# Optimization experiments

Measured on AMD Instinct MI355X. Metric: run time of the kernel, lower is better.

## Reference

```python
import jax, jax.numpy as jnp
import numpy as np

N = 8192  # number of nodes


def _deg_norm(idx, n):
    # degree^{-1/2}, zero-degree clamped to 1 (DGL allow_zero_in_degree behavior)
    deg = jax.ops.segment_sum(jnp.ones(idx.shape[0], jnp.float32), idx, num_segments=n)
    return jax.lax.rsqrt(jnp.maximum(deg, 1.0))


def _graph_conv(h, src, dst, norm_src, norm_dst, W, b):
    # norm='both': scale at src, sparse sum-aggregate, scale at dst, then linear
    h = h * norm_src[:, None]
    m = jax.ops.segment_sum(h[src], dst, num_segments=h.shape[0])  # gather + scatter-add
    m = m * norm_dst[:, None]
    return m @ W + b


def setup_inputs() -> dict:
    key = jax.random.key(0)
    k = jax.random.split(key, 6)
    E = 262144
    x = jax.random.normal(k[0], (N, 256), jnp.float32)
    src = jax.random.randint(k[1], (E,), 0, N, jnp.int32)
    dst = jax.random.randint(k[2], (E,), 0, N, jnp.int32)
    W1 = jax.random.normal(k[3], (256, 128), jnp.float32) * (1.0 / np.sqrt(256))
    b1 = jnp.zeros((128,), jnp.float32)
    W2 = jax.random.normal(k[4], (128, 128), jnp.float32) * (1.0 / np.sqrt(128))
    b2 = jnp.zeros((128,), jnp.float32)
    return {"x": x, "src": src, "dst": dst, "W1": W1, "b1": b1, "W2": W2, "b2": b2}


def reference(x, src, dst, W1, b1, W2, b2):
    n = x.shape[0]
    norm_src = _deg_norm(src, n)  # out-degree norm
    norm_dst = _deg_norm(dst, n)  # in-degree norm
    # encode: GraphConv -> relu -> GraphConv  (dropout=0 -> identity)
    h = jax.nn.relu(_graph_conv(x, src, dst, norm_src, norm_dst, W1, b1))
    h = _graph_conv(h, src, dst, norm_src, norm_dst, W2, b2)
    # decode: sigmoid(h h^T), dense [N, N] reconstruction
    return jax.nn.sigmoid(h @ h.T)
```

## Files before the change

### kernel.cpp

```cpp
#include <hip/hip_runtime.h>
#include <hip/hip_bf16.h>

typedef __attribute__((ext_vector_type(8))) short short8;
typedef __attribute__((ext_vector_type(4))) float f32x4;

#define NNODES 8192
#define FDIM 128

__global__ void k_deg_int(const int* __restrict__ src, const int* __restrict__ dst,
                          int* __restrict__ cnt_s, int* __restrict__ cnt_d, int E) {
    int e = blockIdx.x * blockDim.x + threadIdx.x;
    if (e < E) {
        atomicAdd(&cnt_s[src[e]], 1);
        atomicAdd(&cnt_d[dst[e]], 1);
    }
}

__global__ void k_norms(const int* __restrict__ cnt_s, const int* __restrict__ cnt_d,
                        float* __restrict__ norm_s, float* __restrict__ norm_d, int n) {
    int i = blockIdx.x * blockDim.x + threadIdx.x;
    if (i < n) {
        norm_s[i] = rsqrtf(fmaxf((float)cnt_s[i], 1.0f));
        norm_d[i] = rsqrtf(fmaxf((float)cnt_d[i], 1.0f));
    }
}

__global__ __launch_bounds__(256) void k_scan(const int* __restrict__ cnt,
                                              int* __restrict__ row_start,
                                              int* __restrict__ cursor, int n) {
    __shared__ int partial[256];
    __shared__ int offs[257];
    int t = threadIdx.x;
    int base = t * 32;
    int local[32];
    int s = 0;
#pragma unroll
    for (int i = 0; i < 32; ++i) { local[i] = s; s += cnt[base + i]; }
    partial[t] = s;
    __syncthreads();
    if (t == 0) {
        int acc = 0;
        for (int i = 0; i < 256; ++i) { offs[i] = acc; acc += partial[i]; }
        offs[256] = acc;
    }
    __syncthreads();
    int o = offs[t];
#pragma unroll
    for (int i = 0; i < 32; ++i) {
        int v = o + local[i];
        row_start[base + i] = v;
        cursor[base + i] = v;
    }
    if (t == 0) row_start[n] = offs[256];
}

__global__ void k_fill(const int* __restrict__ src, const int* __restrict__ dst,
                       int* __restrict__ cursor, int* __restrict__ csr_src, int E) {
    int e = blockIdx.x * blockDim.x + threadIdx.x;
    if (e < E) {
        int pos = atomicAdd(&cursor[dst[e]], 1);
        csr_src[pos] = src[e];
    }
}

template<int K, int R>
__global__ void k_linear_norm(const float* __restrict__ X, const float* __restrict__ W,
                              const float* __restrict__ norm, float* __restrict__ Y) {
    int col = threadIdx.x;
    int row0 = blockIdx.x * R;
    float acc[R];
#pragma unroll
    for (int r = 0; r < R; ++r) acc[r] = 0.f;
    for (int k = 0; k < K; ++k) {
        float w = W[k * FDIM + col];
#pragma unroll
        for (int r = 0; r < R; ++r)
            acc[r] = fmaf(X[(size_t)(row0 + r) * K + k], w, acc[r]);
    }
#pragma unroll
    for (int r = 0; r < R; ++r)
        Y[(size_t)(row0 + r) * FDIM + col] = acc[r] * norm[row0 + r];
}

static __device__ inline unsigned short f2bf(float f) {
    union { float f; unsigned int u; } a; a.f = f;
    unsigned int u = a.u;
    unsigned int r = u + 0x7FFFu + ((u >> 16) & 1u);
    return (unsigned short)(r >> 16);
}

template<int MODE>
__global__ __launch_bounds__(256) void k_gather_agg(const float* __restrict__ Y,
                                                    const int* __restrict__ row_start,
                                                    const int* __restrict__ csr_src,
                                                    const float* __restrict__ nd,
                                                    const float* __restrict__ bias,
                                                    void* __restrict__ outp) {
    int t = threadIdx.x;
    int node = blockIdx.x * 8 + (t >> 5);
    int c4 = (t & 31) << 2;
    int beg = row_start[node], end = row_start[node + 1];
    f32x4 acc = {0.f, 0.f, 0.f, 0.f};
    int e = beg;
    for (; e + 1 < end; e += 2) {
        int s0 = csr_src[e], s1 = csr_src[e + 1];
        f32x4 v0 = *(const f32x4*)(Y + ((size_t)s0 << 7) + c4);
        f32x4 v1 = *(const f32x4*)(Y + ((size_t)s1 << 7) + c4);
        acc += v0;
        acc += v1;
    }
    if (e < end) {
        int s0 = csr_src[e];
        acc += *(const f32x4*)(Y + ((size_t)s0 << 7) + c4);
    }
    float scale = nd[node];
    f32x4 b = *(const f32x4*)(bias + c4);
    f32x4 v = acc * scale + b;
    if (MODE == 0) {
#pragma unroll
        for (int i = 0; i < 4; ++i) v[i] = fmaxf(v[i], 0.f);
        *(f32x4*)((float*)outp + ((size_t)node << 7) + c4) = v;
    } else {
        ushort4 u;
        u.x = f2bf(v[0]); u.y = f2bf(v[1]); u.z = f2bf(v[2]); u.w = f2bf(v[3]);
        *(ushort4*)((unsigned short*)outp + ((size_t)node << 7) + c4) = u;
    }
}

__global__ __launch_bounds__(256) void k_decode(const __hip_bfloat16* __restrict__ H,
                                                float* __restrict__ C) {
    __shared__ __align__(16) unsigned char smem[65536];
    unsigned char* sA = smem;
    unsigned char* sB = smem + 32768;
    const int ti = blockIdx.x, tj = blockIdx.y;
    const int t = threadIdx.x;
    const unsigned char* gH = (const unsigned char*)H;

#pragma unroll
    for (int i = 0; i < 8; ++i) {
        int chunk = t + i * 256;
        int row = chunk >> 4;
        int cc = (chunk & 15) << 4;
        int lofs = row * 256 + (cc ^ ((row & 7) << 4));
        *(float4*)(sA + lofs) = *(const float4*)(gH + ((size_t)(ti * 128 + row) << 8) + cc);
        *(float4*)(sB + lofs) = *(const float4*)(gH + ((size_t)(tj * 128 + row) << 8) + cc);
    }
    __syncthreads();

    const int w = t >> 6, lane = t & 63;
    const int wr = (w >> 1) * 64, wc = (w & 1) * 64;
    const int lr = lane & 15;
    const int lk = (lane >> 4) * 16;

    f32x4 acc[4][4] = {};

#pragma unroll
    for (int ks = 0; ks < 4; ++ks) {
        short8 af[4], bfr[4];
#pragma unroll
        for (int mi = 0; mi < 4; ++mi) {
            int row = wr + mi * 16 + lr;
            int off = row * 256 + ((ks * 64 + lk) ^ ((row & 7) << 4));
            af[mi] = *(const short8*)(sA + off);
        }
#pragma unroll
        for (int ni = 0; ni < 4; ++ni) {
            int row = wc + ni * 16 + lr;
            int off = row * 256 + ((ks * 64 + lk) ^ ((row & 7) << 4));
            bfr[ni] = *(const short8*)(sB + off);
        }
#pragma unroll
        for (int mi = 0; mi < 4; ++mi)
#pragma unroll
            for (int ni = 0; ni < 4; ++ni)
                acc[mi][ni] = __builtin_amdgcn_mfma_f32_16x16x32_bf16(af[mi], bfr[ni],
                                                                      acc[mi][ni], 0, 0, 0);
    }

    const int rbase = (lane >> 4) * 4;
    const int cbase = lane & 15;
#pragma unroll
    for (int mi = 0; mi < 4; ++mi) {
#pragma unroll
        for (int ni = 0; ni < 4; ++ni) {
#pragma unroll
            for (int r = 0; r < 4; ++r) {
                int row = ti * 128 + wr + mi * 16 + rbase + r;
                int col = tj * 128 + wc + ni * 16 + cbase;
                float v = acc[mi][ni][r];
                C[(size_t)row * NNODES + col] = 1.0f / (1.0f + __expf(-v));
            }
        }
    }
}

extern "C" void kernel_launch(void* const* d_in, const int* in_sizes, int n_in,
                              void* d_out, int out_size, void* d_ws, size_t ws_size,
                              hipStream_t stream) {
    const float* x  = (const float*)d_in[0];
    const int* src  = (const int*)d_in[1];
    const int* dst  = (const int*)d_in[2];
    const float* W1 = (const float*)d_in[3];
    const float* b1 = (const float*)d_in[4];
    const float* W2 = (const float*)d_in[5];
    const float* b2 = (const float*)d_in[6];
    float* out = (float*)d_out;
    const int E = in_sizes[1];

    char* ws = (char*)d_ws;
    float* norm_s    = (float*)(ws + 0);
    float* norm_d    = (float*)(ws + (32 << 10));
    int*   cnt_s     = (int*)(ws + (64 << 10));
    int*   cnt_d     = (int*)(ws + (96 << 10));
    int*   row_start = (int*)(ws + (128 << 10));
    int*   cursor    = (int*)(ws + (164 << 10));
    int*   csr_src   = (int*)(ws + (196 << 10));
    char*  big       = ws + (196 << 10) + ((size_t)E * 4);
    float* bufA      = (float*)big;
    float* bufB      = (float*)(big + (4 << 20));
    __hip_bfloat16* h2bf = (__hip_bfloat16*)(big + (8 << 20));

    hipMemsetAsync(cnt_s, 0, 64 << 10, stream);

    k_deg_int<<<(E + 255) / 256, 256, 0, stream>>>(src, dst, cnt_s, cnt_d, E);
    k_norms<<<(NNODES + 255) / 256, 256, 0, stream>>>(cnt_s, cnt_d, norm_s, norm_d, NNODES);
    k_scan<<<1, 256, 0, stream>>>(cnt_d, row_start, cursor, NNODES);
    k_fill<<<(E + 255) / 256, 256, 0, stream>>>(src, dst, cursor, csr_src, E);

    k_linear_norm<256, 16><<<NNODES / 16, 128, 0, stream>>>(x, W1, norm_s, bufA);
    k_gather_agg<0><<<NNODES / 8, 256, 0, stream>>>(bufA, row_start, csr_src, norm_d, b1, bufB);

    k_linear_norm<128, 16><<<NNODES / 16, 128, 0, stream>>>(bufB, W2, norm_s, bufA);
    k_gather_agg<1><<<NNODES / 8, 256, 0, stream>>>(bufA, row_start, csr_src, norm_d, b2, h2bf);

    k_decode<<<dim3(64, 64), 256, 0, stream>>>(h2bf, out);
}
```

Baseline: 209.9 us.

## Stage linear inputs in LDS, merge norm into scan, replace memset with kernel

Result: faster. 189.9 us (-9.5%).

```diff
diff --git a/kernel.cpp b/kernel.cpp
--- a/kernel.cpp
+++ b/kernel.cpp
@@ -6,6 +6,11 @@
 
 #define NNODES 8192
 #define FDIM 128
+
+__global__ void k_zero(int* __restrict__ p, int n) {
+    int i = blockIdx.x * blockDim.x + threadIdx.x;
+    if (i < n) p[i] = 0;
+}
 
 __global__ void k_deg_int(const int* __restrict__ src, const int* __restrict__ dst,
                           int* __restrict__ cnt_s, int* __restrict__ cnt_d, int E) {
@@ -16,26 +21,25 @@
     }
 }
 
-__global__ void k_norms(const int* __restrict__ cnt_s, const int* __restrict__ cnt_d,
-                        float* __restrict__ norm_s, float* __restrict__ norm_d, int n) {
-    int i = blockIdx.x * blockDim.x + threadIdx.x;
-    if (i < n) {
-        norm_s[i] = rsqrtf(fmaxf((float)cnt_s[i], 1.0f));
-        norm_d[i] = rsqrtf(fmaxf((float)cnt_d[i], 1.0f));
-    }
-}
-
-__global__ __launch_bounds__(256) void k_scan(const int* __restrict__ cnt,
-                                              int* __restrict__ row_start,
-                                              int* __restrict__ cursor, int n) {
+__global__ __launch_bounds__(256) void k_scan_norms(const int* __restrict__ cnt_s,
+                                                    const int* __restrict__ cnt_d,
+                                                    float* __restrict__ norm_s,
+                                                    float* __restrict__ norm_d,
+                                                    int* __restrict__ row_start,
+                                                    int* __restrict__ cursor, int n) {
     __shared__ int partial[256];
     __shared__ int offs[257];
     int t = threadIdx.x;
     int base = t * 32;
+#pragma unroll
+    for (int i = 0; i < 32; ++i) {
+        norm_s[base + i] = rsqrtf(fmaxf((float)cnt_s[base + i], 1.0f));
+        norm_d[base + i] = rsqrtf(fmaxf((float)cnt_d[base + i], 1.0f));
+    }
     int local[32];
     int s = 0;
 #pragma unroll
-    for (int i = 0; i < 32; ++i) { local[i] = s; s += cnt[base + i]; }
+    for (int i = 0; i < 32; ++i) { local[i] = s; s += cnt_d[base + i]; }
     partial[t] = s;
     __syncthreads();
     if (t == 0) {
@@ -63,23 +67,41 @@
     }
 }
 
-template<int K, int R>
-__global__ void k_linear_norm(const float* __restrict__ X, const float* __restrict__ W,
-                              const float* __restrict__ norm, float* __restrict__ Y) {
-    int col = threadIdx.x;
-    int row0 = blockIdx.x * R;
-    float acc[R];
-#pragma unroll
-    for (int r = 0; r < R; ++r) acc[r] = 0.f;
-    for (int k = 0; k < K; ++k) {
-        float w = W[k * FDIM + col];
-#pragma unroll
-        for (int r = 0; r < R; ++r)
-            acc[r] = fmaf(X[(size_t)(row0 + r) * K + k], w, acc[r]);
-    }
-#pragma unroll
-    for (int r = 0; r < R; ++r)
-        Y[(size_t)(row0 + r) * FDIM + col] = acc[r] * norm[row0 + r];
+template<int K>
+__global__ __launch_bounds__(256) void k_linear(const float* __restrict__ X,
+                                                const float* __restrict__ W,
+                                                const float* __restrict__ norm,
+                                                float* __restrict__ Y) {
+    __shared__ float xs[16][K];
+    int t = threadIdx.x;
+    int row0 = blockIdx.x * 16;
+    constexpr int K4 = K / 4;
+    constexpr int NCH = 16 * K4 / 256;
+#pragma unroll
+    for (int i = 0; i < NCH; ++i) {
+        int c = t + i * 256;
+        int r = c / K4, k4 = c % K4;
+        *(float4*)&xs[r][k4 * 4] = *(const float4*)(X + (size_t)(row0 + r) * K + k4 * 4);
+    }
+    __syncthreads();
+
+    int lane = t & 31, g = t >> 5;
+    int r0 = g * 2, r1 = g * 2 + 1;
+    int c = lane * 4;
+    f32x4 acc0 = {0.f, 0.f, 0.f, 0.f}, acc1 = {0.f, 0.f, 0.f, 0.f};
+    for (int k = 0; k < K; k += 4) {
+        f32x4 x0 = *(f32x4*)&xs[r0][k];
+        f32x4 x1 = *(f32x4*)&xs[r1][k];
+#pragma unroll
+        for (int kk = 0; kk < 4; ++kk) {
+            f32x4 w = *(const f32x4*)(W + (size_t)(k + kk) * FDIM + c);
+            acc0 += w * x0[kk];
+            acc1 += w * x1[kk];
+        }
+    }
+    float n0 = norm[row0 + r0], n1 = norm[row0 + r1];
+    *(f32x4*)(Y + (size_t)(row0 + r0) * FDIM + c) = acc0 * n0;
+    *(f32x4*)(Y + (size_t)(row0 + r1) * FDIM + c) = acc1 * n1;
 }
 
 static __device__ inline unsigned short f2bf(float f) {
@@ -220,17 +242,16 @@
     float* bufB      = (float*)(big + (4 << 20));
     __hip_bfloat16* h2bf = (__hip_bfloat16*)(big + (8 << 20));
 
-    hipMemsetAsync(cnt_s, 0, 64 << 10, stream);
+    k_zero<<<(2 * NNODES + 255) / 256, 256, 0, stream>>>(cnt_s, 2 * NNODES);
 
     k_deg_int<<<(E + 255) / 256, 256, 0, stream>>>(src, dst, cnt_s, cnt_d, E);
-    k_norms<<<(NNODES + 255) / 256, 256, 0, stream>>>(cnt_s, cnt_d, norm_s, norm_d, NNODES);
-    k_scan<<<1, 256, 0, stream>>>(cnt_d, row_start, cursor, NNODES);
+    k_scan_norms<<<1, 256, 0, stream>>>(cnt_s, cnt_d, norm_s, norm_d, row_start, cursor, NNODES);
     k_fill<<<(E + 255) / 256, 256, 0, stream>>>(src, dst, cursor, csr_src, E);
 
-    k_linear_norm<256, 16><<<NNODES / 16, 128, 0, stream>>>(x, W1, norm_s, bufA);
+    k_linear<256><<<NNODES / 16, 256, 0, stream>>>(x, W1, norm_s, bufA);
     k_gather_agg<0><<<NNODES / 8, 256, 0, stream>>>(bufA, row_start, csr_src, norm_d, b1, bufB);
 
-    k_linear_norm<128, 16><<<NNODES / 16, 128, 0, stream>>>(bufB, W2, norm_s, bufA);
+    k_linear<128><<<NNODES / 16, 256, 0, stream>>>(bufB, W2, norm_s, bufA);
     k_gather_agg<1><<<NNODES / 8, 256, 0, stream>>>(bufA, row_start, csr_src, norm_d, b2, h2bf);
 
     k_decode<<<dim3(64, 64), 256, 0, stream>>>(h2bf, out);
```
